# Performance work log

Hardware: AMD Instinct MI355X
Metric: run time of the kernel (lower is better)

## Reference

```python
import jax, jax.numpy as jnp
import numpy as np

TOP_K = 2
NOISE_STDDEV = 1.0


def setup_inputs() -> dict:
    key = jax.random.key(0)
    k1, k2, k3, k4 = jax.random.split(key, 4)
    N, D, E = 16384, 2048, 64
    x = jax.random.normal(k1, (N, D), dtype=jnp.float32)
    W_gate = jax.random.normal(k2, (E, D), dtype=jnp.float32) * (1.0 / np.sqrt(D))
    W_noise = jax.random.normal(k3, (E, D), dtype=jnp.float32) * (1.0 / np.sqrt(D))
    noise = jax.random.normal(k4, (N, E), dtype=jnp.float32)
    return {"x": x, "W_gate": W_gate, "W_noise": W_noise, "noise": noise}


def reference(x, W_gate, W_noise, noise):
    # clean gating logits: [N, E]
    clean_logits = jnp.einsum("nd,ed->ne", x, W_gate)
    # noise scale via softplus of second projection (training mode)
    noise_scale = jax.nn.softplus(jnp.einsum("nd,ed->ne", x, W_noise))
    noisy_logits = clean_logits + noise_scale * noise * NOISE_STDDEV
    # top-k selection then softmax over the k selected logits
    top_k_logits, top_k_indices = jax.lax.top_k(noisy_logits, TOP_K)
    combined_weights = jax.nn.softmax(top_k_logits, axis=-1)
    return (combined_weights, top_k_indices, clean_logits)
```

## Files before the change

kernel.cpp:

```cpp
#include <hip/hip_runtime.h>
#include <math.h>


constexpr int NROWS = 16384;
constexpr int DDIM  = 2048;
constexpr int EDIM  = 64;
constexpr int BM    = 32;
constexpr int NKS   = 64;
constexpr int LSTR  = 132;
constexpr int IDX_OFF   = NROWS * 2;
constexpr int CLEAN_OFF = NROWS * 4;
constexpr size_t WPACK = 262144;
constexpr int XBUF  = 4096;
constexpr int NBUF  = 4;
constexpr int LDSSZ = 17408;

typedef _Float16 f16x8 __attribute__((ext_vector_type(8)));
typedef float    f32x4 __attribute__((ext_vector_type(4)));

__device__ __forceinline__ float softplus_f(float z) {
    return fmaxf(z, 0.0f) + log1pf(expf(-fabsf(z)));
}

__device__ __forceinline__ void gload16(const void* g, void* l) {
    __builtin_amdgcn_global_load_lds(
        (const __attribute__((address_space(1))) unsigned int*)g,
        (__attribute__((address_space(3))) unsigned int*)l, 16, 0, 0);
}

__global__ __launch_bounds__(256) void split_w_kernel(
    const float* __restrict__ Wg, const float* __restrict__ Wn,
    _Float16* __restrict__ wh, _Float16* __restrict__ wl)
{
    const int t    = blockIdx.x * 256 + threadIdx.x;
    const int grp  = t >> 6;
    const int lane = t & 63;
    const int kc   = grp >> 3;
    const int cg   = (grp >> 1) & 3;
    const int cf   = grp & 1;
    const int col  = cg * 32 + cf * 16 + (lane & 15);
    const int k0   = kc * 32 + (lane >> 4) * 8;
    const float* src = (col < 64) ? &Wg[(size_t)col * DDIM + k0]
                                  : &Wn[(size_t)(col - 64) * DDIM + k0];
    const float4 v0 = *reinterpret_cast<const float4*>(src);
    const float4 v1 = *reinterpret_cast<const float4*>(src + 4);
    float vv[8] = {v0.x, v0.y, v0.z, v0.w, v1.x, v1.y, v1.z, v1.w};
    union { _Float16 h[8]; uint4 u; } hh, ll;
    #pragma unroll
    for (int j = 0; j < 8; ++j) {
        hh.h[j] = (_Float16)vv[j];
        ll.h[j] = (_Float16)((vv[j] - (float)hh.h[j]) * 2048.0f);
    }
    const size_t off = (size_t)grp * 512 + lane * 8;
    *reinterpret_cast<uint4*>(&wh[off]) = hh.u;
    *reinterpret_cast<uint4*>(&wl[off]) = ll.u;
}

__device__ __forceinline__ void split8(const float4 a, const float4 b, f16x8& h, f16x8& l) {
    const float v[8] = {a.x, a.y, a.z, a.w, b.x, b.y, b.z, b.w};
    #pragma unroll
    for (int j = 0; j < 8; ++j) {
        const _Float16 hh = (_Float16)v[j];
        h[j] = hh;
        l[j] = (_Float16)((v[j] - (float)hh) * 2048.0f);
    }
}

__global__ __launch_bounds__(256, 2) void gating_mfma_kernel(
    const float* __restrict__ x,
    const float* __restrict__ noise,
    const _Float16* __restrict__ whp,
    const _Float16* __restrict__ wlp,
    float* __restrict__ out)
{
    extern __shared__ __align__(16) unsigned char smem[];

    const int tid = threadIdx.x;
    const int row_base = blockIdx.x * BM;
    const int lane = tid & 63;
    const int cg   = tid >> 6;
    const int g    = (lane >> 4) & 3;
    const int idx  = lane & 15;

    const int sr  = tid >> 3;
    const int sq  = tid & 7;
    const int sq2 = sq ^ (sr & 7);
    const float* xsrc = x + (size_t)(row_base + sr) * DDIM + sq2 * 4;

    const _Float16* bh = whp + (size_t)cg * 1024 + lane * 8;
    const _Float16* bl = wlp + (size_t)cg * 1024 + lane * 8;

    int aoff[2][2];
    #pragma unroll
    for (int rf = 0; rf < 2; ++rf) {
        const int row = rf * 16 + idx;
        #pragma unroll
        for (int j = 0; j < 2; ++j)
            aoff[rf][j] = row * 128 + (((g * 2 + j) ^ (row & 7)) << 4);
    }

    f32x4 accm[2][2], accc[2][2];
    #pragma unroll
    for (int rf = 0; rf < 2; ++rf)
        #pragma unroll
        for (int cf = 0; cf < 2; ++cf) { accm[rf][cf] = (f32x4)0.0f; accc[rf][cf] = (f32x4)0.0f; }

    auto stageX = [&](int u) {
        gload16(xsrc + u * 32, smem + (u & (NBUF - 1)) * XBUF + tid * 16);
    };
    auto loadW = [&](int u, float4& h0, float4& h1, float4& l0, float4& l1) {
        const _Float16* ph = bh + (size_t)u * 4096;
        const _Float16* pl = bl + (size_t)u * 4096;
        h0 = *reinterpret_cast<const float4*>(ph);
        h1 = *reinterpret_cast<const float4*>(ph + 512);
        l0 = *reinterpret_cast<const float4*>(pl);
        l1 = *reinterpret_cast<const float4*>(pl + 512);
    };

    auto compute = [&](int t, const float4& h0, const float4& h1,
                       const float4& l0, const float4& l1) {
        const int b = (t & (NBUF - 1)) * XBUF;
        const float4 a00 = *reinterpret_cast<const float4*>(&smem[b + aoff[0][0]]);
        const float4 a01 = *reinterpret_cast<const float4*>(&smem[b + aoff[0][1]]);
        const float4 a10 = *reinterpret_cast<const float4*>(&smem[b + aoff[1][0]]);
        const float4 a11 = *reinterpret_cast<const float4*>(&smem[b + aoff[1][1]]);
        const f16x8 Bh0 = __builtin_bit_cast(f16x8, h0);
        const f16x8 Bh1 = __builtin_bit_cast(f16x8, h1);
        const f16x8 Bl0 = __builtin_bit_cast(f16x8, l0);
        const f16x8 Bl1 = __builtin_bit_cast(f16x8, l1);

        f16x8 Ah0, Al0, Ah1, Al1;
        split8(a00, a01, Ah0, Al0);
        split8(a10, a11, Ah1, Al1);

        accm[0][0] = __builtin_amdgcn_mfma_f32_16x16x32_f16(Ah0, Bh0, accm[0][0], 0, 0, 0);
        accm[0][1] = __builtin_amdgcn_mfma_f32_16x16x32_f16(Ah0, Bh1, accm[0][1], 0, 0, 0);
        accm[1][0] = __builtin_amdgcn_mfma_f32_16x16x32_f16(Ah1, Bh0, accm[1][0], 0, 0, 0);
        accm[1][1] = __builtin_amdgcn_mfma_f32_16x16x32_f16(Ah1, Bh1, accm[1][1], 0, 0, 0);
        accc[0][0] = __builtin_amdgcn_mfma_f32_16x16x32_f16(Al0, Bh0, accc[0][0], 0, 0, 0);
        accc[0][1] = __builtin_amdgcn_mfma_f32_16x16x32_f16(Al0, Bh1, accc[0][1], 0, 0, 0);
        accc[1][0] = __builtin_amdgcn_mfma_f32_16x16x32_f16(Al1, Bh0, accc[1][0], 0, 0, 0);
        accc[1][1] = __builtin_amdgcn_mfma_f32_16x16x32_f16(Al1, Bh1, accc[1][1], 0, 0, 0);
        accc[0][0] = __builtin_amdgcn_mfma_f32_16x16x32_f16(Ah0, Bl0, accc[0][0], 0, 0, 0);
        accc[0][1] = __builtin_amdgcn_mfma_f32_16x16x32_f16(Ah0, Bl1, accc[0][1], 0, 0, 0);
        accc[1][0] = __builtin_amdgcn_mfma_f32_16x16x32_f16(Ah1, Bl0, accc[1][0], 0, 0, 0);
        accc[1][1] = __builtin_amdgcn_mfma_f32_16x16x32_f16(Ah1, Bl1, accc[1][1], 0, 0, 0);
    };

    float4 s0h0, s0h1, s0l0, s0l1, s1h0, s1h1, s1l0, s1l1;

    stageX(0); loadW(0, s0h0, s0h1, s0l0, s0l1);
    stageX(1); loadW(1, s1h0, s1h1, s1l0, s1l1);
    __builtin_amdgcn_sched_barrier(0);

    for (int tt = 0; tt < 31; ++tt) {
        const int t0 = 2 * tt;
        stageX(t0 + 2);
        asm volatile("s_waitcnt vmcnt(6)" ::: "memory");
        __builtin_amdgcn_s_barrier();
        __builtin_amdgcn_sched_barrier(0);
        compute(t0, s0h0, s0h1, s0l0, s0l1);
        loadW(t0 + 2, s0h0, s0h1, s0l0, s0l1);
        __builtin_amdgcn_sched_barrier(0);
        stageX(t0 + 3);
        asm volatile("s_waitcnt vmcnt(6)" ::: "memory");
        __builtin_amdgcn_s_barrier();
        __builtin_amdgcn_sched_barrier(0);
        compute(t0 + 1, s1h0, s1h1, s1l0, s1l1);
        loadW(t0 + 3, s1h0, s1h1, s1l0, s1l1);
        __builtin_amdgcn_sched_barrier(0);
    }
    asm volatile("s_waitcnt vmcnt(5)" ::: "memory");
    __builtin_amdgcn_s_barrier();
    __builtin_amdgcn_sched_barrier(0);
    compute(62, s0h0, s0h1, s0l0, s0l1);
    asm volatile("s_waitcnt vmcnt(0)" ::: "memory");
    __builtin_amdgcn_s_barrier();
    __builtin_amdgcn_sched_barrier(0);
    compute(63, s1h0, s1h1, s1l0, s1l1);

    __builtin_amdgcn_s_barrier();

    float* L = reinterpret_cast<float*>(smem);
    #pragma unroll
    for (int rf = 0; rf < 2; ++rf)
        #pragma unroll
        for (int cf = 0; cf < 2; ++cf) {
            const int col = cg * 32 + cf * 16 + idx;
            #pragma unroll
            for (int q = 0; q < 4; ++q) {
                const int lrow = rf * 16 + g * 4 + q;
                L[lrow * LSTR + col] = accm[rf][cf][q] + accc[rf][cf][q] * 4.8828125e-4f;
            }
        }
    __syncthreads();

    {
        const int row = tid >> 3;
        const int j   = tid & 7;
        const int e0  = j * 8;
        const int grow = row_base + row;

        const float4 c0 = *reinterpret_cast<const float4*>(&L[row * LSTR + e0]);
        const float4 c1 = *reinterpret_cast<const float4*>(&L[row * LSTR + e0 + 4]);
        const float4 s0 = *reinterpret_cast<const float4*>(&L[row * LSTR + 64 + e0]);
        const float4 s1 = *reinterpret_cast<const float4*>(&L[row * LSTR + 64 + e0 + 4]);
        *reinterpret_cast<float4*>(&out[CLEAN_OFF + (size_t)grow * EDIM + e0])     = c0;
        *reinterpret_cast<float4*>(&out[CLEAN_OFF + (size_t)grow * EDIM + e0 + 4]) = c1;

        const float4 z0 = *reinterpret_cast<const float4*>(&noise[(size_t)grow * EDIM + e0]);
        const float4 z1 = *reinterpret_cast<const float4*>(&noise[(size_t)grow * EDIM + e0 + 4]);

        float nv[8];
        nv[0] = fmaf(softplus_f(s0.x), z0.x, c0.x);
        nv[1] = fmaf(softplus_f(s0.y), z0.y, c0.y);
        nv[2] = fmaf(softplus_f(s0.z), z0.z, c0.z);
        nv[3] = fmaf(softplus_f(s0.w), z0.w, c0.w);
        nv[4] = fmaf(softplus_f(s1.x), z1.x, c1.x);
        nv[5] = fmaf(softplus_f(s1.y), z1.y, c1.y);
        nv[6] = fmaf(softplus_f(s1.z), z1.z, c1.z);
        nv[7] = fmaf(softplus_f(s1.w), z1.w, c1.w);

        float v0 = nv[0], v1 = -INFINITY;
        int   i0 = e0,    i1 = -1;
        #pragma unroll
        for (int m = 1; m < 8; ++m) {
            const float v = nv[m]; const int e = e0 + m;
            if (v > v0)      { v1 = v0; i1 = i0; v0 = v; i0 = e; }
            else if (v > v1) { v1 = v;  i1 = e; }
        }
        #pragma unroll
        for (int d = 1; d < 8; d <<= 1) {
            const float ov0 = __shfl_xor(v0, d); const int oi0 = __shfl_xor(i0, d);
            const float ov1 = __shfl_xor(v1, d); const int oi1 = __shfl_xor(i1, d);
            const bool aFirst = (v0 > ov0) || (v0 == ov0 && i0 < oi0);
            float n0, n1; int ni0, ni1;
            if (aFirst) {
                n0 = v0; ni0 = i0;
                const bool s = (v1 > ov0) || (v1 == ov0 && i1 < oi0);
                n1 = s ? v1 : ov0; ni1 = s ? i1 : oi0;
            } else {
                n0 = ov0; ni0 = oi0;
                const bool s = (ov1 > v0) || (ov1 == v0 && oi1 < i0);
                n1 = s ? ov1 : v0; ni1 = s ? oi1 : i0;
            }
            v0 = n0; i0 = ni0; v1 = n1; i1 = ni1;
        }
        if (j == 0) {
            const float ex = expf(v1 - v0);
            const float w0 = 1.0f / (1.0f + ex);
            const float w1 = 1.0f - w0;
            out[(size_t)grow * 2 + 0] = w0;
            out[(size_t)grow * 2 + 1] = w1;
            out[IDX_OFF + (size_t)grow * 2 + 0] = (float)i0;
            out[IDX_OFF + (size_t)grow * 2 + 1] = (float)i1;
        }
    }
}

extern "C" void kernel_launch(void* const* d_in, const int* in_sizes, int n_in,
                              void* d_out, int out_size, void* d_ws, size_t ws_size,
                              hipStream_t stream) {
    const float* x     = (const float*)d_in[0];
    const float* Wg    = (const float*)d_in[1];
    const float* Wn    = (const float*)d_in[2];
    const float* noise = (const float*)d_in[3];
    float* out = (float*)d_out;

    _Float16* wh = (_Float16*)d_ws;
    _Float16* wl = wh + WPACK;

    split_w_kernel<<<dim3(128), dim3(256), 0, stream>>>(Wg, Wn, wh, wl);
    gating_mfma_kernel<<<dim3(NROWS / BM), dim3(256), LDSSZ, stream>>>(x, noise, wh, wl, out);
}
```

Baseline: 55.60 us.

## Split the K dimension in two with 1024-thread tiles and a separate reduce/top-k kernel

The fused GEMM-plus-top-k kernel is split in two. The GEMM kernel now processes 128-row tiles with 16 waves per block, and each block handles one half of the 2048-wide reduction, giving 256 blocks. Partial logits go to a global workspace buffer. A new kernel sums the two halves, writes the clean logits, and does the softplus, noise, top-2 and softmax. The goal is more weight reuse per block and shorter per-block K loops, at the cost of an extra kernel launch and a round trip of partial results through global memory.

New measurement: 51.17 us, median of 2. 8.0% less time.

```diff
diff --git a/kernel.cpp b/kernel.cpp
--- a/kernel.cpp
+++ b/kernel.cpp
@@ -5,15 +5,13 @@
 constexpr int NROWS = 16384;
 constexpr int DDIM  = 2048;
 constexpr int EDIM  = 64;
-constexpr int BM    = 32;
-constexpr int NKS   = 64;
-constexpr int LSTR  = 132;
+constexpr int BM    = 128;
+constexpr int NKS   = 32;
 constexpr int IDX_OFF   = NROWS * 2;
 constexpr int CLEAN_OFF = NROWS * 4;
 constexpr size_t WPACK = 262144;
-constexpr int XBUF  = 4096;
+constexpr int XS    = 16384;
 constexpr int NBUF  = 4;
-constexpr int LDSSZ = 17408;
 
 typedef _Float16 f16x8 __attribute__((ext_vector_type(8)));
 typedef float    f32x4 __attribute__((ext_vector_type(4)));
@@ -66,37 +64,40 @@
     }
 }
 
-__global__ __launch_bounds__(256, 2) void gating_mfma_kernel(
+__global__ __launch_bounds__(1024, 4) void gemm_part_kernel(
     const float* __restrict__ x,
-    const float* __restrict__ noise,
     const _Float16* __restrict__ whp,
     const _Float16* __restrict__ wlp,
-    float* __restrict__ out)
+    float* __restrict__ pbuf)
 {
     extern __shared__ __align__(16) unsigned char smem[];
 
-    const int tid = threadIdx.x;
-    const int row_base = blockIdx.x * BM;
+    const int tid  = threadIdx.x;
     const int lane = tid & 63;
-    const int cg   = tid >> 6;
+    const int wid  = tid >> 6;
+    const int rg   = wid >> 2;
+    const int cg   = wid & 3;
     const int g    = (lane >> 4) & 3;
     const int idx  = lane & 15;
+    const int kh   = blockIdx.x >> 7;
+    const int rt   = blockIdx.x & 127;
+    const int row_base = rt * BM;
 
     const int sr  = tid >> 3;
     const int sq  = tid & 7;
     const int sq2 = sq ^ (sr & 7);
-    const float* xsrc = x + (size_t)(row_base + sr) * DDIM + sq2 * 4;
-
-    const _Float16* bh = whp + (size_t)cg * 1024 + lane * 8;
-    const _Float16* bl = wlp + (size_t)cg * 1024 + lane * 8;
+    const float* xsrc = x + (size_t)(row_base + sr) * DDIM + kh * 1024 + sq2 * 4;
+
+    const char* bh2 = (const char*)whp + (size_t)kh * 262144 + (cg * 2) * 1024 + lane * 16;
+    const char* bl2 = (const char*)wlp + (size_t)kh * 262144 + (cg * 2) * 1024 + lane * 16;
 
     int aoff[2][2];
     #pragma unroll
     for (int rf = 0; rf < 2; ++rf) {
-        const int row = rf * 16 + idx;
+        const int row = rg * 32 + rf * 16 + idx;
         #pragma unroll
         for (int j = 0; j < 2; ++j)
-            aoff[rf][j] = row * 128 + (((g * 2 + j) ^ (row & 7)) << 4);
+            aoff[rf][j] = row * 128 + (((2 * g + j) ^ (row & 7)) << 4);
     }
 
     f32x4 accm[2][2], accc[2][2];
@@ -106,20 +107,20 @@
         for (int cf = 0; cf < 2; ++cf) { accm[rf][cf] = (f32x4)0.0f; accc[rf][cf] = (f32x4)0.0f; }
 
     auto stageX = [&](int u) {
-        gload16(xsrc + u * 32, smem + (u & (NBUF - 1)) * XBUF + tid * 16);
+        gload16(xsrc + u * 32, smem + (u & (NBUF - 1)) * XS + tid * 16);
     };
     auto loadW = [&](int u, float4& h0, float4& h1, float4& l0, float4& l1) {
-        const _Float16* ph = bh + (size_t)u * 4096;
-        const _Float16* pl = bl + (size_t)u * 4096;
+        const char* ph = bh2 + (size_t)u * 8192;
+        const char* pl = bl2 + (size_t)u * 8192;
         h0 = *reinterpret_cast<const float4*>(ph);
-        h1 = *reinterpret_cast<const float4*>(ph + 512);
+        h1 = *reinterpret_cast<const float4*>(ph + 1024);
         l0 = *reinterpret_cast<const float4*>(pl);
-        l1 = *reinterpret_cast<const float4*>(pl + 512);
+        l1 = *reinterpret_cast<const float4*>(pl + 1024);
     };
 
     auto compute = [&](int t, const float4& h0, const float4& h1,
                        const float4& l0, const float4& l1) {
-        const int b = (t & (NBUF - 1)) * XBUF;
+        const int b = (t & (NBUF - 1)) * XS;
         const float4 a00 = *reinterpret_cast<const float4*>(&smem[b + aoff[0][0]]);
         const float4 a01 = *reinterpret_cast<const float4*>(&smem[b + aoff[0][1]]);
         const float4 a10 = *reinterpret_cast<const float4*>(&smem[b + aoff[1][0]]);
@@ -153,7 +154,7 @@
     stageX(1); loadW(1, s1h0, s1h1, s1l0, s1l1);
     __builtin_amdgcn_sched_barrier(0);
 
-    for (int tt = 0; tt < 31; ++tt) {
+    for (int tt = 0; tt < 15; ++tt) {
         const int t0 = 2 * tt;
         stageX(t0 + 2);
         asm volatile("s_waitcnt vmcnt(6)" ::: "memory");
@@ -173,15 +174,13 @@
     asm volatile("s_waitcnt vmcnt(5)" ::: "memory");
     __builtin_amdgcn_s_barrier();
     __builtin_amdgcn_sched_barrier(0);
-    compute(62, s0h0, s0h1, s0l0, s0l1);
+    compute(30, s0h0, s0h1, s0l0, s0l1);
     asm volatile("s_waitcnt vmcnt(0)" ::: "memory");
     __builtin_amdgcn_s_barrier();
     __builtin_amdgcn_sched_barrier(0);
-    compute(63, s1h0, s1h1, s1l0, s1l1);
-
-    __builtin_amdgcn_s_barrier();
-
-    float* L = reinterpret_cast<float*>(smem);
+    compute(31, s1h0, s1h1, s1l0, s1l1);
+
+    float* dst = pbuf + (size_t)kh * NROWS * 128;
     #pragma unroll
     for (int rf = 0; rf < 2; ++rf)
         #pragma unroll
@@ -189,72 +188,89 @@
             const int col = cg * 32 + cf * 16 + idx;
             #pragma unroll
             for (int q = 0; q < 4; ++q) {
-                const int lrow = rf * 16 + g * 4 + q;
-                L[lrow * LSTR + col] = accm[rf][cf][q] + accc[rf][cf][q] * 4.8828125e-4f;
+                const int lrow = rg * 32 + rf * 16 + g * 4 + q;
+                dst[(size_t)(row_base + lrow) * 128 + col] =
+                    accm[rf][cf][q] + accc[rf][cf][q] * 4.8828125e-4f;
             }
         }
-    __syncthreads();
-
-    {
-        const int row = tid >> 3;
-        const int j   = tid & 7;
-        const int e0  = j * 8;
-        const int grow = row_base + row;
-
-        const float4 c0 = *reinterpret_cast<const float4*>(&L[row * LSTR + e0]);
-        const float4 c1 = *reinterpret_cast<const float4*>(&L[row * LSTR + e0 + 4]);
-        const float4 s0 = *reinterpret_cast<const float4*>(&L[row * LSTR + 64 + e0]);
-        const float4 s1 = *reinterpret_cast<const float4*>(&L[row * LSTR + 64 + e0 + 4]);
-        *reinterpret_cast<float4*>(&out[CLEAN_OFF + (size_t)grow * EDIM + e0])     = c0;
-        *reinterpret_cast<float4*>(&out[CLEAN_OFF + (size_t)grow * EDIM + e0 + 4]) = c1;
-
-        const float4 z0 = *reinterpret_cast<const float4*>(&noise[(size_t)grow * EDIM + e0]);
-        const float4 z1 = *reinterpret_cast<const float4*>(&noise[(size_t)grow * EDIM + e0 + 4]);
-
-        float nv[8];
-        nv[0] = fmaf(softplus_f(s0.x), z0.x, c0.x);
-        nv[1] = fmaf(softplus_f(s0.y), z0.y, c0.y);
-        nv[2] = fmaf(softplus_f(s0.z), z0.z, c0.z);
-        nv[3] = fmaf(softplus_f(s0.w), z0.w, c0.w);
-        nv[4] = fmaf(softplus_f(s1.x), z1.x, c1.x);
-        nv[5] = fmaf(softplus_f(s1.y), z1.y, c1.y);
-        nv[6] = fmaf(softplus_f(s1.z), z1.z, c1.z);
-        nv[7] = fmaf(softplus_f(s1.w), z1.w, c1.w);
-
-        float v0 = nv[0], v1 = -INFINITY;
-        int   i0 = e0,    i1 = -1;
-        #pragma unroll
-        for (int m = 1; m < 8; ++m) {
-            const float v = nv[m]; const int e = e0 + m;
-            if (v > v0)      { v1 = v0; i1 = i0; v0 = v; i0 = e; }
-            else if (v > v1) { v1 = v;  i1 = e; }
+}
+
+__global__ __launch_bounds__(256) void reduce_topk_kernel(
+    const float* __restrict__ pbuf,
+    const float* __restrict__ noise,
+    float* __restrict__ out)
+{
+    const int tid = threadIdx.x;
+    const int row = tid >> 3;
+    const int j   = tid & 7;
+    const int e0  = j * 8;
+    const int grow = blockIdx.x * 32 + row;
+
+    const float* p0 = pbuf + (size_t)grow * 128;
+    const float* p1 = pbuf + (size_t)(NROWS + grow) * 128;
+
+    float4 c0 = *reinterpret_cast<const float4*>(&p0[e0]);
+    float4 c1 = *reinterpret_cast<const float4*>(&p0[e0 + 4]);
+    float4 s0 = *reinterpret_cast<const float4*>(&p0[64 + e0]);
+    float4 s1 = *reinterpret_cast<const float4*>(&p0[64 + e0 + 4]);
+    const float4 d0 = *reinterpret_cast<const float4*>(&p1[e0]);
+    const float4 d1 = *reinterpret_cast<const float4*>(&p1[e0 + 4]);
+    const float4 t0 = *reinterpret_cast<const float4*>(&p1[64 + e0]);
+    const float4 t1 = *reinterpret_cast<const float4*>(&p1[64 + e0 + 4]);
+    c0.x += d0.x; c0.y += d0.y; c0.z += d0.z; c0.w += d0.w;
+    c1.x += d1.x; c1.y += d1.y; c1.z += d1.z; c1.w += d1.w;
+    s0.x += t0.x; s0.y += t0.y; s0.z += t0.z; s0.w += t0.w;
+    s1.x += t1.x; s1.y += t1.y; s1.z += t1.z; s1.w += t1.w;
+
+    *reinterpret_cast<float4*>(&out[CLEAN_OFF + (size_t)grow * EDIM + e0])     = c0;
+    *reinterpret_cast<float4*>(&out[CLEAN_OFF + (size_t)grow * EDIM + e0 + 4]) = c1;
+
+    const float4 z0 = *reinterpret_cast<const float4*>(&noise[(size_t)grow * EDIM + e0]);
+    const float4 z1 = *reinterpret_cast<const float4*>(&noise[(size_t)grow * EDIM + e0 + 4]);
+
+    float nv[8];
+    nv[0] = fmaf(softplus_f(s0.x), z0.x, c0.x);
+    nv[1] = fmaf(softplus_f(s0.y), z0.y, c0.y);
+    nv[2] = fmaf(softplus_f(s0.z), z0.z, c0.z);
+    nv[3] = fmaf(softplus_f(s0.w), z0.w, c0.w);
+    nv[4] = fmaf(softplus_f(s1.x), z1.x, c1.x);
+    nv[5] = fmaf(softplus_f(s1.y), z1.y, c1.y);
+    nv[6] = fmaf(softplus_f(s1.z), z1.z, c1.z);
+    nv[7] = fmaf(softplus_f(s1.w), z1.w, c1.w);
+
+    float v0 = nv[0], v1 = -INFINITY;
+    int   i0 = e0,    i1 = -1;
+    #pragma unroll
+    for (int m = 1; m < 8; ++m) {
+        const float v = nv[m]; const int e = e0 + m;
+        if (v > v0)      { v1 = v0; i1 = i0; v0 = v; i0 = e; }
+        else if (v > v1) { v1 = v;  i1 = e; }
+    }
+    #pragma unroll
+    for (int d = 1; d < 8; d <<= 1) {
+        const float ov0 = __shfl_xor(v0, d); const int oi0 = __shfl_xor(i0, d);
+        const float ov1 = __shfl_xor(v1, d); const int oi1 = __shfl_xor(i1, d);
+        const bool aFirst = (v0 > ov0) || (v0 == ov0 && i0 < oi0);
+        float n0, n1; int ni0, ni1;
+        if (aFirst) {
+            n0 = v0; ni0 = i0;
+            const bool s = (v1 > ov0) || (v1 == ov0 && i1 < oi0);
+            n1 = s ? v1 : ov0; ni1 = s ? i1 : oi0;
+        } else {
+            n0 = ov0; ni0 = oi0;
+            const bool s = (ov1 > v0) || (ov1 == v0 && oi1 < i0);
+            n1 = s ? ov1 : v0; ni1 = s ? oi1 : i0;
         }
-        #pragma unroll
-        for (int d = 1; d < 8; d <<= 1) {
-            const float ov0 = __shfl_xor(v0, d); const int oi0 = __shfl_xor(i0, d);
-            const float ov1 = __shfl_xor(v1, d); const int oi1 = __shfl_xor(i1, d);
-            const bool aFirst = (v0 > ov0) || (v0 == ov0 && i0 < oi0);
-            float n0, n1; int ni0, ni1;
-            if (aFirst) {
-                n0 = v0; ni0 = i0;
-                const bool s = (v1 > ov0) || (v1 == ov0 && i1 < oi0);
-                n1 = s ? v1 : ov0; ni1 = s ? i1 : oi0;
-            } else {
-                n0 = ov0; ni0 = oi0;
-                const bool s = (ov1 > v0) || (ov1 == v0 && oi1 < i0);
-                n1 = s ? ov1 : v0; ni1 = s ? oi1 : i0;
-            }
-            v0 = n0; i0 = ni0; v1 = n1; i1 = ni1;
-        }
-        if (j == 0) {
-            const float ex = expf(v1 - v0);
-            const float w0 = 1.0f / (1.0f + ex);
-            const float w1 = 1.0f - w0;
-            out[(size_t)grow * 2 + 0] = w0;
-            out[(size_t)grow * 2 + 1] = w1;
-            out[IDX_OFF + (size_t)grow * 2 + 0] = (float)i0;
-            out[IDX_OFF + (size_t)grow * 2 + 1] = (float)i1;
-        }
+        v0 = n0; i0 = ni0; v1 = n1; i1 = ni1;
+    }
+    if (j == 0) {
+        const float ex = expf(v1 - v0);
+        const float w0 = 1.0f / (1.0f + ex);
+        const float w1 = 1.0f - w0;
+        out[(size_t)grow * 2 + 0] = w0;
+        out[(size_t)grow * 2 + 1] = w1;
+        out[IDX_OFF + (size_t)grow * 2 + 0] = (float)i0;
+        out[IDX_OFF + (size_t)grow * 2 + 1] = (float)i1;
     }
 }
 
@@ -269,7 +285,9 @@
 
     _Float16* wh = (_Float16*)d_ws;
     _Float16* wl = wh + WPACK;
+    float* pbuf  = (float*)((char*)d_ws + (1 << 20));
 
     split_w_kernel<<<dim3(128), dim3(256), 0, stream>>>(Wg, Wn, wh, wl);
-    gating_mfma_kernel<<<dim3(NROWS / BM), dim3(256), LDSSZ, stream>>>(x, noise, wh, wl, out);
-}
+    gemm_part_kernel<<<dim3(256), dim3(1024), NBUF * XS, stream>>>(x, wh, wl, pbuf);
+    reduce_topk_kernel<<<dim3(NROWS / 32), dim3(256), 0, stream>>>(pbuf, noise, out);
+}
```

## Widen gating GEMM tile to 64 rows with 16 waves per block

Applied to the files above, without the earlier changes.

The block tile grows from 32 to 64 rows and the block from 256 to 1024 threads, arranged as 4 row-groups by 4 column-groups of waves. Each wave now computes one 16-row by 32-column fragment, so it issues fewer MFMAs per step, and each block stages 64 rows of x per K-step. The first 8 waves issue the x loads and all waves load their own W fragments, with wave-dependent waitcnt values. The aim is more waves per CU to hide latency, at the cost of more per-wave W loads relative to compute and more barrier overhead across 16 waves.

Result: slower. 57.58 us (+3.6%).

```diff
diff --git a/kernel.cpp b/kernel.cpp
--- a/kernel.cpp
+++ b/kernel.cpp
@@ -5,15 +5,15 @@
 constexpr int NROWS = 16384;
 constexpr int DDIM  = 2048;
 constexpr int EDIM  = 64;
-constexpr int BM    = 32;
+constexpr int BM    = 64;
 constexpr int NKS   = 64;
 constexpr int LSTR  = 132;
 constexpr int IDX_OFF   = NROWS * 2;
 constexpr int CLEAN_OFF = NROWS * 4;
 constexpr size_t WPACK = 262144;
-constexpr int XBUF  = 4096;
+constexpr int XS    = 8192;
 constexpr int NBUF  = 4;
-constexpr int LDSSZ = 17408;
+constexpr int LDSSZ = 33792;
 
 typedef _Float16 f16x8 __attribute__((ext_vector_type(8)));
 typedef float    f32x4 __attribute__((ext_vector_type(4)));
@@ -66,7 +66,7 @@
     }
 }
 
-__global__ __launch_bounds__(256, 2) void gating_mfma_kernel(
+__global__ __launch_bounds__(1024, 4) void gating_mfma_kernel(
     const float* __restrict__ x,
     const float* __restrict__ noise,
     const _Float16* __restrict__ whp,
@@ -75,76 +75,67 @@
 {
     extern __shared__ __align__(16) unsigned char smem[];
 
-    const int tid = threadIdx.x;
-    const int row_base = blockIdx.x * BM;
+    const int tid  = threadIdx.x;
     const int lane = tid & 63;
-    const int cg   = tid >> 6;
+    const int wid  = tid >> 6;
+    const int rg   = wid >> 2;
+    const int cg   = wid & 3;
     const int g    = (lane >> 4) & 3;
     const int idx  = lane & 15;
-
-    const int sr  = tid >> 3;
+    const int row_base = blockIdx.x * BM;
+
+    const int sr  = (tid >> 3) & 63;
     const int sq  = tid & 7;
     const int sq2 = sq ^ (sr & 7);
     const float* xsrc = x + (size_t)(row_base + sr) * DDIM + sq2 * 4;
 
-    const _Float16* bh = whp + (size_t)cg * 1024 + lane * 8;
-    const _Float16* bl = wlp + (size_t)cg * 1024 + lane * 8;
-
-    int aoff[2][2];
-    #pragma unroll
-    for (int rf = 0; rf < 2; ++rf) {
-        const int row = rf * 16 + idx;
+    const char* bh2 = (const char*)whp + (cg * 2) * 1024 + lane * 16;
+    const char* bl2 = (const char*)wlp + (cg * 2) * 1024 + lane * 16;
+
+    int aoff[2];
+    {
+        const int row = rg * 16 + idx;
         #pragma unroll
         for (int j = 0; j < 2; ++j)
-            aoff[rf][j] = row * 128 + (((g * 2 + j) ^ (row & 7)) << 4);
-    }
-
-    f32x4 accm[2][2], accc[2][2];
-    #pragma unroll
-    for (int rf = 0; rf < 2; ++rf)
-        #pragma unroll
-        for (int cf = 0; cf < 2; ++cf) { accm[rf][cf] = (f32x4)0.0f; accc[rf][cf] = (f32x4)0.0f; }
+            aoff[j] = row * 128 + (((2 * g + j) ^ (row & 7)) << 4);
+    }
+
+    f32x4 accm[2], accc[2];
+    accm[0] = (f32x4)0.0f; accm[1] = (f32x4)0.0f;
+    accc[0] = (f32x4)0.0f; accc[1] = (f32x4)0.0f;
 
     auto stageX = [&](int u) {
-        gload16(xsrc + u * 32, smem + (u & (NBUF - 1)) * XBUF + tid * 16);
+        if (wid < 8)
+            gload16(xsrc + u * 32, smem + (u & (NBUF - 1)) * XS + tid * 16);
     };
     auto loadW = [&](int u, float4& h0, float4& h1, float4& l0, float4& l1) {
-        const _Float16* ph = bh + (size_t)u * 4096;
-        const _Float16* pl = bl + (size_t)u * 4096;
+        const char* ph = bh2 + (size_t)u * 8192;
+        const char* pl = bl2 + (size_t)u * 8192;
         h0 = *reinterpret_cast<const float4*>(ph);
-        h1 = *reinterpret_cast<const float4*>(ph + 512);
+        h1 = *reinterpret_cast<const float4*>(ph + 1024);
         l0 = *reinterpret_cast<const float4*>(pl);
-        l1 = *reinterpret_cast<const float4*>(pl + 512);
+        l1 = *reinterpret_cast<const float4*>(pl + 1024);
     };
 
     auto compute = [&](int t, const float4& h0, const float4& h1,
                        const float4& l0, const float4& l1) {
-        const int b = (t & (NBUF - 1)) * XBUF;
-        const float4 a00 = *reinterpret_cast<const float4*>(&smem[b + aoff[0][0]]);
-        const float4 a01 = *reinterpret_cast<const float4*>(&smem[b + aoff[0][1]]);
-        const float4 a10 = *reinterpret_cast<const float4*>(&smem[b + aoff[1][0]]);
-        const float4 a11 = *reinterpret_cast<const float4*>(&smem[b + aoff[1][1]]);
+        const int b = (t & (NBUF - 1)) * XS;
+        const float4 a0 = *reinterpret_cast<const float4*>(&smem[b + aoff[0]]);
+        const float4 a1 = *reinterpret_cast<const float4*>(&smem[b + aoff[1]]);
         const f16x8 Bh0 = __builtin_bit_cast(f16x8, h0);
         const f16x8 Bh1 = __builtin_bit_cast(f16x8, h1);
         const f16x8 Bl0 = __builtin_bit_cast(f16x8, l0);
         const f16x8 Bl1 = __builtin_bit_cast(f16x8, l1);
 
-        f16x8 Ah0, Al0, Ah1, Al1;
-        split8(a00, a01, Ah0, Al0);
-        split8(a10, a11, Ah1, Al1);
-
-        accm[0][0] = __builtin_amdgcn_mfma_f32_16x16x32_f16(Ah0, Bh0, accm[0][0], 0, 0, 0);
-        accm[0][1] = __builtin_amdgcn_mfma_f32_16x16x32_f16(Ah0, Bh1, accm[0][1], 0, 0, 0);
-        accm[1][0] = __builtin_amdgcn_mfma_f32_16x16x32_f16(Ah1, Bh0, accm[1][0], 0, 0, 0);
-        accm[1][1] = __builtin_amdgcn_mfma_f32_16x16x32_f16(Ah1, Bh1, accm[1][1], 0, 0, 0);
-        accc[0][0] = __builtin_amdgcn_mfma_f32_16x16x32_f16(Al0, Bh0, accc[0][0], 0, 0, 0);
-        accc[0][1] = __builtin_amdgcn_mfma_f32_16x16x32_f16(Al0, Bh1, accc[0][1], 0, 0, 0);
-        accc[1][0] = __builtin_amdgcn_mfma_f32_16x16x32_f16(Al1, Bh0, accc[1][0], 0, 0, 0);
-        accc[1][1] = __builtin_amdgcn_mfma_f32_16x16x32_f16(Al1, Bh1, accc[1][1], 0, 0, 0);
-        accc[0][0] = __builtin_amdgcn_mfma_f32_16x16x32_f16(Ah0, Bl0, accc[0][0], 0, 0, 0);
-        accc[0][1] = __builtin_amdgcn_mfma_f32_16x16x32_f16(Ah0, Bl1, accc[0][1], 0, 0, 0);
-        accc[1][0] = __builtin_amdgcn_mfma_f32_16x16x32_f16(Ah1, Bl0, accc[1][0], 0, 0, 0);
-        accc[1][1] = __builtin_amdgcn_mfma_f32_16x16x32_f16(Ah1, Bl1, accc[1][1], 0, 0, 0);
+        f16x8 Ah, Al;
+        split8(a0, a1, Ah, Al);
+
+        accm[0] = __builtin_amdgcn_mfma_f32_16x16x32_f16(Ah, Bh0, accm[0], 0, 0, 0);
+        accm[1] = __builtin_amdgcn_mfma_f32_16x16x32_f16(Ah, Bh1, accm[1], 0, 0, 0);
+        accc[0] = __builtin_amdgcn_mfma_f32_16x16x32_f16(Al, Bh0, accc[0], 0, 0, 0);
+        accc[1] = __builtin_amdgcn_mfma_f32_16x16x32_f16(Al, Bh1, accc[1], 0, 0, 0);
+        accc[0] = __builtin_amdgcn_mfma_f32_16x16x32_f16(Ah, Bl0, accc[0], 0, 0, 0);
+        accc[1] = __builtin_amdgcn_mfma_f32_16x16x32_f16(Ah, Bl1, accc[1], 0, 0, 0);
     };
 
     float4 s0h0, s0h1, s0l0, s0l1, s1h0, s1h1, s1l0, s1l1;
@@ -156,21 +147,24 @@
     for (int tt = 0; tt < 31; ++tt) {
         const int t0 = 2 * tt;
         stageX(t0 + 2);
-        asm volatile("s_waitcnt vmcnt(6)" ::: "memory");
+        if (wid < 8) asm volatile("s_waitcnt vmcnt(6)" ::: "memory");
+        else         asm volatile("s_waitcnt vmcnt(4)" ::: "memory");
         __builtin_amdgcn_s_barrier();
         __builtin_amdgcn_sched_barrier(0);
         compute(t0, s0h0, s0h1, s0l0, s0l1);
         loadW(t0 + 2, s0h0, s0h1, s0l0, s0l1);
         __builtin_amdgcn_sched_barrier(0);
         stageX(t0 + 3);
-        asm volatile("s_waitcnt vmcnt(6)" ::: "memory");
+        if (wid < 8) asm volatile("s_waitcnt vmcnt(6)" ::: "memory");
+        else         asm volatile("s_waitcnt vmcnt(4)" ::: "memory");
         __builtin_amdgcn_s_barrier();
         __builtin_amdgcn_sched_barrier(0);
         compute(t0 + 1, s1h0, s1h1, s1l0, s1l1);
         loadW(t0 + 3, s1h0, s1h1, s1l0, s1l1);
         __builtin_amdgcn_sched_barrier(0);
     }
-    asm volatile("s_waitcnt vmcnt(5)" ::: "memory");
+    if (wid < 8) asm volatile("s_waitcnt vmcnt(5)" ::: "memory");
+    else         asm volatile("s_waitcnt vmcnt(4)" ::: "memory");
     __builtin_amdgcn_s_barrier();
     __builtin_amdgcn_sched_barrier(0);
     compute(62, s0h0, s0h1, s0l0, s0l1);
@@ -179,23 +173,21 @@
     __builtin_amdgcn_sched_barrier(0);
     compute(63, s1h0, s1h1, s1l0, s1l1);
 
-    __builtin_amdgcn_s_barrier();
+    __syncthreads();
 
     float* L = reinterpret_cast<float*>(smem);
     #pragma unroll
-    for (int rf = 0; rf < 2; ++rf)
-        #pragma unroll
-        for (int cf = 0; cf < 2; ++cf) {
-            const int col = cg * 32 + cf * 16 + idx;
-            #pragma unroll
-            for (int q = 0; q < 4; ++q) {
-                const int lrow = rf * 16 + g * 4 + q;
-                L[lrow * LSTR + col] = accm[rf][cf][q] + accc[rf][cf][q] * 4.8828125e-4f;
-            }
-        }
+    for (int cf = 0; cf < 2; ++cf) {
+        const int col = cg * 32 + cf * 16 + idx;
+        #pragma unroll
+        for (int q = 0; q < 4; ++q) {
+            const int lrow = rg * 16 + g * 4 + q;
+            L[lrow * LSTR + col] = accm[cf][q] + accc[cf][q] * 4.8828125e-4f;
+        }
+    }
     __syncthreads();
 
-    {
+    if (tid < 512) {
         const int row = tid >> 3;
         const int j   = tid & 7;
         const int e0  = j * 8;
@@ -271,5 +263,5 @@
     _Float16* wl = wh + WPACK;
 
     split_w_kernel<<<dim3(128), dim3(256), 0, stream>>>(Wg, Wn, wh, wl);
-    gating_mfma_kernel<<<dim3(NROWS / BM), dim3(256), LDSSZ, stream>>>(x, noise, wh, wl, out);
-}
+    gating_mfma_kernel<<<dim3(NROWS / BM), dim3(1024), LDSSZ, stream>>>(x, noise, wh, wl, out);
+}
```
